# Performance work log

Measured on AMD Instinct MI355X. Metric: run time of the kernel, lower is better.

Reference implementation:

```python
import jax, jax.numpy as jnp
import numpy as np


def setup_inputs() -> dict:
    key = jax.random.key(0)
    k1, k2 = jax.random.split(key)
    B, N, C, S = 4, 16384, 128, 32
    # normalized point coordinates in [-1, 1]
    ptcloud = jax.random.uniform(k1, (B, N, 3), jnp.float32, -1.0, 1.0)
    cubic_features = jax.random.normal(k2, (B, C, S, S, S), jnp.float32)
    return {"ptcloud": ptcloud, "cubic_features": cubic_features, "neighborhood_size": 1}


def reference(ptcloud, cubic_features, neighborhood_size):
    # ptcloud: [B, N, 3] in [-1, 1]; cubic_features: [B, C, S, S, S]
    B, C, S = cubic_features.shape[0], cubic_features.shape[1], cubic_features.shape[2]
    N = ptcloud.shape[1]
    h = S / 2.0
    pt = ptcloud * h + h  # scaled to [0, S]
    ns = neighborhood_size - 1
    lower = jnp.floor(pt).astype(jnp.int32)  # [B, N, 3]
    # CUDA kernel: upper = ceil(pt); if lower == upper: upper += 1 -> upper == lower + 1 always;
    # vertices range over [lower - ns, upper + ns] => 2*neighborhood_size values per axis
    offs = jnp.arange(-ns, ns + 2, dtype=jnp.int32)  # K = 2*neighborhood_size
    idx3 = lower[:, :, None, :] + offs[None, None, :, None]  # [B, N, K, 3]
    ii, jj, kk = idx3[..., 0], idx3[..., 1], idx3[..., 2]
    # cartesian product of per-axis candidates -> [B, N, K, K, K]
    I = ii[:, :, :, None, None]
    J = jj[:, :, None, :, None]
    Kz = kk[:, :, None, None, :]
    valid = (I >= 0) & (I < S) & (J >= 0) & (J < S) & (Kz >= 0) & (Kz < S)
    flat = (jnp.clip(I, 0, S - 1) * S + jnp.clip(J, 0, S - 1)) * S + jnp.clip(Kz, 0, S - 1)
    K = offs.shape[0]
    V = K * K * K  # vertices per point
    flat = flat.reshape(B, N, V)
    valid = valid.reshape(B, N, V)
    cf = cubic_features.reshape(B, C, S * S * S)
    gathered = jax.vmap(lambda f, i: f[:, i])(cf, flat)  # [B, C, N, V]
    point_features = jnp.transpose(gathered, (0, 2, 3, 1)) * valid[..., None].astype(cubic_features.dtype)
    return point_features  # [B, N, V, C]
```

## Files before the change

### kernel.cpp

```cpp
#include <hip/hip_runtime.h>
#include <hip/hip_bf16.h>

#define PB 4
#define PN 16384
#define PC 128
#define PS 32
#define PS3 32768
#define PV 8
#define NBKT (PB * 32 * 32)
#define CAP 128

typedef float f32x4 __attribute__((ext_vector_type(4)));

__device__ __forceinline__ ushort bf16_rne(float f) {
    uint u = __float_as_uint(f);
    u += 0x7FFFu + ((u >> 16) & 1u);
    return (ushort)(u >> 16);
}

__device__ __forceinline__ void lower_of(const float* __restrict__ pt, int bn,
                                         int& li, int& lj, int& lk) {
    li = (int)floorf(__fadd_rn(__fmul_rn(pt[(size_t)bn * 3 + 0], 16.f), 16.f));
    lj = (int)floorf(__fadd_rn(__fmul_rn(pt[(size_t)bn * 3 + 1], 16.f), 16.f));
    lk = (int)floorf(__fadd_rn(__fmul_rn(pt[(size_t)bn * 3 + 2], 16.f), 16.f));
}

__global__ __launch_bounds__(256) void cfs_bucket_kernel(
        const float* __restrict__ pt, uint* __restrict__ cur,
        uint* __restrict__ list) {
    const int bn = blockIdx.x * 256 + threadIdx.x;
    if (bn >= PB * PN) return;
    int li, lj, lk;
    lower_of(pt, bn, li, lj, lk);
    const int b  = bn >> 14;
    const int i0 = min(max(li, 0), 31);
    const int j0 = min(max(lj, 0), 31);
    const int q  = (b << 10) | (i0 << 5) | j0;
    const uint pos = atomicAdd(&cur[q], 1u);
    if (pos < CAP) list[(size_t)q * CAP + pos] = (uint)bn;
}

__global__ __launch_bounds__(256) void cfs_bucket_gather_kernel(
        const float* __restrict__ pt, const float* __restrict__ cf,
        const uint* __restrict__ cur, const uint* __restrict__ list,
        float* __restrict__ out) {
    __shared__ __attribute__((aligned(16))) ushort win[4][32][132];
    __shared__ int4 spt[CAP];
    const int w = blockIdx.x;
    const int q = (w & 7) * 512 + (w >> 3);
    const int n = min((int)cur[q], CAP);
    if (n == 0) return;

    const int b  = q >> 10;
    const int i0 = (q >> 5) & 31;
    const int j0 = q & 31;
    const float* cfb = cf + (size_t)b * PC * PS3;
    const int t = threadIdx.x;

    if (t < n) {
        const int bn = (int)list[(size_t)q * CAP + t];
        int li, lj, lk;
        lower_of(pt, bn, li, lj, lk);
        spt[t] = make_int4(li, lj, lk, bn);
    }

    #pragma unroll
    for (int it = 0; it < 16; ++it) {
        const int L   = it * 256 + t;
        const int row = L >> 10;
        const int ch  = (L >> 3) & 127;
        const int pos = L & 7;
        const int ii  = min(i0 + (row >> 1), 31);
        const int jj  = min(j0 + (row & 1), 31);
        f32x4 a = *reinterpret_cast<const f32x4*>(
            cfb + (size_t)ch * PS3 + (ii * 32 + jj) * 32 + pos * 4);
        win[row][pos * 4 + 0][ch] = bf16_rne(a.x);
        win[row][pos * 4 + 1][ch] = bf16_rne(a.y);
        win[row][pos * 4 + 2][ch] = bf16_rne(a.z);
        win[row][pos * 4 + 3][ch] = bf16_rne(a.w);
    }
    __syncthreads();

    const int v   = t >> 5;
    const int cl  = t & 31;
    const int di  = v >> 2, dj = (v >> 1) & 1, dk = v & 1;
    const int row = v >> 1;

    #pragma unroll 2
    for (int idx = 0; idx < n; ++idx) {
        const int4 pp = spt[idx];
        const int ii = pp.x + di, jj = pp.y + dj, kk = pp.z + dk;
        const bool ok = ((unsigned)ii < 32u) & ((unsigned)jj < 32u) &
                        ((unsigned)kk < 32u);
        const float m = ok ? 1.0f : 0.0f;
        const int kidx = min(max(kk, 0), 31);
        const unsigned long long wv =
            *reinterpret_cast<const unsigned long long*>(&win[row][kidx][cl * 4]);
        f32x4 r;
        r.x = __uint_as_float(((uint)(wv       ) & 0xffffu) << 16) * m;
        r.y = __uint_as_float(((uint)(wv >> 16 ) & 0xffffu) << 16) * m;
        r.z = __uint_as_float(((uint)(wv >> 32 ) & 0xffffu) << 16) * m;
        r.w = __uint_as_float(((uint)(wv >> 48 ) & 0xffffu) << 16) * m;
        __builtin_nontemporal_store(
            r, reinterpret_cast<f32x4*>(out + (size_t)pp.w * (PV * PC)) +
                   v * 32 + cl);
    }
}

__global__ void cfs_gather_d_kernel(const float* __restrict__ pt,
                                    const float* __restrict__ cf,
                                    float* __restrict__ out) {
    const int bn = blockIdx.x;
    const int b  = bn >> 14;
    const int t  = threadIdx.x;
    const int v  = t >> 5;
    const int c4 = (t & 31) << 2;

    int li, lj, lk;
    lower_of(pt, bn, li, lj, lk);
    const int ii = li + ((v >> 2) & 1);
    const int jj = lj + ((v >> 1) & 1);
    const int kk = lk + (v & 1);
    const bool ok = ((unsigned)ii < 32u) & ((unsigned)jj < 32u) &
                    ((unsigned)kk < 32u);
    const int flat = (min(max(ii, 0), 31) * 32 + min(max(jj, 0), 31)) * 32 +
                     min(max(kk, 0), 31);

    f32x4 r = (f32x4)(0.f);
    if (ok) {
        const float* basep = cf + (size_t)b * PC * PS3 + flat;
        r.x = basep[(size_t)(c4 + 0) * PS3];
        r.y = basep[(size_t)(c4 + 1) * PS3];
        r.z = basep[(size_t)(c4 + 2) * PS3];
        r.w = basep[(size_t)(c4 + 3) * PS3];
    }
    *(reinterpret_cast<f32x4*>(out) + (size_t)bn * 256 + t) = r;
}

extern "C" void kernel_launch(void* const* d_in, const int* in_sizes, int n_in,
                              void* d_out, int out_size, void* d_ws, size_t ws_size,
                              hipStream_t stream) {
    const float* pt = (const float*)d_in[0];
    const float* cf = (const float*)d_in[1];
    float* out = (float*)d_out;

    const size_t needed = (size_t)NBKT * 4 + (size_t)NBKT * CAP * 4;
    if (d_ws != nullptr && ws_size >= needed) {
        uint* cur  = (uint*)d_ws;
        uint* list = cur + NBKT;
        (void)hipMemsetAsync(cur, 0, (size_t)NBKT * 4, stream);
        cfs_bucket_kernel<<<dim3(PB * PN / 256), dim3(256), 0, stream>>>(
            pt, cur, list);
        cfs_bucket_gather_kernel<<<dim3(NBKT), dim3(256), 0, stream>>>(
            pt, cf, cur, list, out);
    } else {
        cfs_gather_d_kernel<<<dim3(PB * PN), dim3(256), 0, stream>>>(pt, cf, out);
    }
}
```

Baseline: 71.01 us.

## Group 2x2 buckets per block with shared 3x3 row window

Each block now handles a 2x2 group of (i,j) buckets and loads a 3x3 set of rows into LDS, where each bucket used to load its own 2x2 rows. This cuts redundant global reads of feature rows from 4 per bucket to 2.25, and it uses 512-thread blocks with two points handled in parallel. Point coordinates are packed into a uint2 to save shared memory. In exchange, LDS use per block is larger (about 76KB), which may lower occupancy, and there are fewer blocks.

```diff
diff --git a/kernel.cpp b/kernel.cpp
--- a/kernel.cpp
+++ b/kernel.cpp
@@ -9,6 +9,7 @@
 #define PV 8
 #define NBKT (PB * 32 * 32)
 #define CAP 128
+#define NBG (PB * 16 * 16)
 
 typedef float f32x4 __attribute__((ext_vector_type(4)));
 
@@ -40,70 +41,88 @@
     if (pos < CAP) list[(size_t)q * CAP + pos] = (uint)bn;
 }
 
-__global__ __launch_bounds__(256) void cfs_bucket_gather_kernel(
+__global__ __launch_bounds__(512) void cfs_group_gather_kernel(
         const float* __restrict__ pt, const float* __restrict__ cf,
         const uint* __restrict__ cur, const uint* __restrict__ list,
         float* __restrict__ out) {
-    __shared__ __attribute__((aligned(16))) ushort win[4][32][132];
-    __shared__ int4 spt[CAP];
-    const int w = blockIdx.x;
-    const int q = (w & 7) * 512 + (w >> 3);
-    const int n = min((int)cur[q], CAP);
-    if (n == 0) return;
+    __shared__ __attribute__((aligned(16))) ushort win[9][32][132];
+    __shared__ uint2 spt[512];
 
-    const int b  = q >> 10;
-    const int i0 = (q >> 5) & 31;
-    const int j0 = q & 31;
-    const float* cfb = cf + (size_t)b * PC * PS3;
-    const int t = threadIdx.x;
+    const int w  = blockIdx.x;
+    const int g  = (w & 7) * (NBG / 8) + (w >> 3);
+    const int b  = g >> 8;
+    const int gi = (g >> 4) & 15;
+    const int gj = g & 15;
+    const int t  = threadIdx.x;
 
-    if (t < n) {
-        const int bn = (int)list[(size_t)q * CAP + t];
+    int pu[4], m = 0;
+    #pragma unroll
+    for (int u = 0; u < 4; ++u) {
+        const int q = (b << 10) | ((2 * gi + (u >> 1)) << 5) | (2 * gj + (u & 1));
+        pu[u] = m;
+        m += min((int)cur[q], CAP);
+    }
+    if (m == 0) return;
+
+    if (t < m) {
+        const int u = (t >= pu[1]) + (t >= pu[2]) + (t >= pu[3]);
+        const int q = (b << 10) | ((2 * gi + (u >> 1)) << 5) | (2 * gj + (u & 1));
+        const int bn = (int)list[(size_t)q * CAP + (t - pu[u])];
         int li, lj, lk;
         lower_of(pt, bn, li, lj, lk);
-        spt[t] = make_int4(li, lj, lk, bn);
+        spt[t] = make_uint2((uint)(li + 16) | ((uint)(lj + 16) << 8) |
+                            ((uint)(lk + 16) << 16), (uint)bn);
     }
 
+    const float* cfb = cf + (size_t)b * PC * PS3;
     #pragma unroll
-    for (int it = 0; it < 16; ++it) {
-        const int L   = it * 256 + t;
-        const int row = L >> 10;
-        const int ch  = (L >> 3) & 127;
-        const int pos = L & 7;
-        const int ii  = min(i0 + (row >> 1), 31);
-        const int jj  = min(j0 + (row & 1), 31);
-        f32x4 a = *reinterpret_cast<const f32x4*>(
-            cfb + (size_t)ch * PS3 + (ii * 32 + jj) * 32 + pos * 4);
-        win[row][pos * 4 + 0][ch] = bf16_rne(a.x);
-        win[row][pos * 4 + 1][ch] = bf16_rne(a.y);
-        win[row][pos * 4 + 2][ch] = bf16_rne(a.z);
-        win[row][pos * 4 + 3][ch] = bf16_rne(a.w);
+    for (int row = 0; row < 9; ++row) {
+        const int ii = min(2 * gi + row / 3, 31);
+        const int jj = min(2 * gj + row % 3, 31);
+        const float* rp = cfb + (size_t)(ii * 32 + jj) * 32;
+        #pragma unroll
+        for (int e = 0; e < 2; ++e) {
+            const int x   = e * 512 + t;
+            const int ch  = x >> 3;
+            const int pos = x & 7;
+            f32x4 a = *reinterpret_cast<const f32x4*>(
+                rp + (size_t)ch * PS3 + pos * 4);
+            win[row][pos * 4 + 0][ch] = bf16_rne(a.x);
+            win[row][pos * 4 + 1][ch] = bf16_rne(a.y);
+            win[row][pos * 4 + 2][ch] = bf16_rne(a.z);
+            win[row][pos * 4 + 3][ch] = bf16_rne(a.w);
+        }
     }
     __syncthreads();
 
-    const int v   = t >> 5;
-    const int cl  = t & 31;
-    const int di  = v >> 2, dj = (v >> 1) & 1, dk = v & 1;
-    const int row = v >> 1;
+    const int s  = t >> 8;
+    const int v  = (t >> 5) & 7;
+    const int cl = t & 31;
+    const int di = v >> 2, dj = (v >> 1) & 1, dk = v & 1;
 
     #pragma unroll 2
-    for (int idx = 0; idx < n; ++idx) {
-        const int4 pp = spt[idx];
-        const int ii = pp.x + di, jj = pp.y + dj, kk = pp.z + dk;
+    for (int idx = s; idx < m; idx += 2) {
+        const uint2 pp = spt[idx];
+        const int li = (int)(pp.x & 0xffu) - 16;
+        const int lj = (int)((pp.x >> 8) & 0xffu) - 16;
+        const int lk = (int)((pp.x >> 16) & 0xffu) - 16;
+        const int ii = li + di, jj = lj + dj, kk = lk + dk;
         const bool ok = ((unsigned)ii < 32u) & ((unsigned)jj < 32u) &
                         ((unsigned)kk < 32u);
-        const float m = ok ? 1.0f : 0.0f;
-        const int kidx = min(max(kk, 0), 31);
+        const float mm = ok ? 1.0f : 0.0f;
+        const int ri = min(max(ii, 0), 31) - 2 * gi;
+        const int rj = min(max(jj, 0), 31) - 2 * gj;
+        const int kq = min(max(kk, 0), 31);
         const unsigned long long wv =
-            *reinterpret_cast<const unsigned long long*>(&win[row][kidx][cl * 4]);
+            *reinterpret_cast<const unsigned long long*>(
+                &win[ri * 3 + rj][kq][cl * 4]);
         f32x4 r;
-        r.x = __uint_as_float(((uint)(wv       ) & 0xffffu) << 16) * m;
-        r.y = __uint_as_float(((uint)(wv >> 16 ) & 0xffffu) << 16) * m;
-        r.z = __uint_as_float(((uint)(wv >> 32 ) & 0xffffu) << 16) * m;
-        r.w = __uint_as_float(((uint)(wv >> 48 ) & 0xffffu) << 16) * m;
+        r.x = __uint_as_float(((uint)(wv      ) & 0xffffu) << 16) * mm;
+        r.y = __uint_as_float(((uint)(wv >> 16) & 0xffffu) << 16) * mm;
+        r.z = __uint_as_float(((uint)(wv >> 32) & 0xffffu) << 16) * mm;
+        r.w = __uint_as_float(((uint)(wv >> 48) & 0xffffu) << 16) * mm;
         __builtin_nontemporal_store(
-            r, reinterpret_cast<f32x4*>(out + (size_t)pp.w * (PV * PC)) +
-                   v * 32 + cl);
+            r, reinterpret_cast<f32x4*>(out) + (size_t)pp.y * 256 + v * 32 + cl);
     }
 }
 
@@ -151,7 +170,7 @@
         (void)hipMemsetAsync(cur, 0, (size_t)NBKT * 4, stream);
         cfs_bucket_kernel<<<dim3(PB * PN / 256), dim3(256), 0, stream>>>(
             pt, cur, list);
-        cfs_bucket_gather_kernel<<<dim3(NBKT), dim3(256), 0, stream>>>(
+        cfs_group_gather_kernel<<<dim3(NBG), dim3(512), 0, stream>>>(
             pt, cf, cur, list, out);
     } else {
         cfs_gather_d_kernel<<<dim3(PB * PN), dim3(256), 0, stream>>>(pt, cf, out);
```

Measured after the change: 74.18 us. +4.5%, slower.
